# Kernel tuning notes

Measured on AMD Instinct MI355X. Metric: run time of the kernel, lower is better.

The kernel has to match this reference:

```python
import jax, jax.numpy as jnp
import numpy as np

N_NODES = 50000
N_EDGES = 800000
N_REL = 8
DIM = 256


def setup_inputs() -> dict:
    key = jax.random.key(0)
    ks = jax.random.split(key, 6)
    x = jax.random.normal(ks[0], (N_NODES, DIM), dtype=jnp.float32)
    # xavier-uniform-ish scale for [R, in, out] weights
    limit = float(np.sqrt(6.0 / (DIM + DIM)))
    W0 = jax.random.uniform(ks[1], (N_REL, DIM, DIM), dtype=jnp.float32, minval=-limit, maxval=limit)
    W1 = jax.random.uniform(ks[2], (N_REL, DIM, DIM), dtype=jnp.float32, minval=-limit, maxval=limit)
    b0 = jnp.zeros((DIM,), dtype=jnp.float32)
    b1 = jnp.zeros((DIM,), dtype=jnp.float32)
    edge_index = jax.random.randint(ks[3], (2, N_EDGES), 0, N_NODES, dtype=jnp.int64)
    edge_type = jax.random.randint(ks[4], (N_EDGES,), 0, N_REL, dtype=jnp.int64)
    return {"x": x, "W0": W0, "b0": b0, "W1": W1, "b1": b1,
            "edge_index": edge_index, "edge_type": edge_type}


def _rgcn_layer(x, W, b, src, dst, edge_type, num_nodes):
    # grouped GEMM over all relations: [R, N, out]
    xt = jnp.einsum('ni,rio->rno', x, W)
    # per-edge message = relu(x[src] @ W[edge_type] + b)  -> [E, out]
    msg = jax.nn.relu(xt[edge_type, src] + b)
    # scatter-add into destination nodes
    return jax.ops.segment_sum(msg, dst, num_segments=num_nodes)


def reference(x, W0, b0, W1, b1, edge_index, edge_type):
    src, dst = edge_index[0], edge_index[1]
    h = _rgcn_layer(x, W0, b0, src, dst, edge_type, x.shape[0])
    h = _rgcn_layer(h, W1, b1, src, dst, edge_type, x.shape[0])
    return h
```

## Files before the change

### kernel.cpp

```cpp
#include <hip/hip_runtime.h>

#define DIM 256
#define N_REL 8

typedef __attribute__((ext_vector_type(8))) short short8_t;
typedef __attribute__((ext_vector_type(4))) float float4_t;

__device__ inline unsigned short f2bf(float f) {
    unsigned u = __float_as_uint(f);
    u += 0x7FFFu + ((u >> 16) & 1u);
    return (unsigned short)(u >> 16);
}
__device__ inline float bf2f(unsigned short h) {
    return __uint_as_float(((unsigned)h) << 16);
}

__global__ __launch_bounds__(256) void cast_f32_bf16(
    const float* __restrict__ in, unsigned short* __restrict__ out, int n4)
{
    const int i = blockIdx.x * blockDim.x + threadIdx.x;
    if (i >= n4) return;
    const float4 v = ((const float4*)in)[i];
    ushort4 o;
    o.x = f2bf(v.x); o.y = f2bf(v.y); o.z = f2bf(v.z); o.w = f2bf(v.w);
    ((ushort4*)out)[i] = o;
}

__global__ __launch_bounds__(256) void transpose_cast_w(
    const float* __restrict__ W, unsigned short* __restrict__ Wt)
{
    __shared__ float tile[32][33];
    const int rel = blockIdx.z;
    const int i0 = blockIdx.x * 32, o0 = blockIdx.y * 32;
    const int tx = threadIdx.x, ty = threadIdx.y;
    const float* Wr = W + (size_t)rel * DIM * DIM;
    unsigned short* Wtr = Wt + (size_t)rel * DIM * DIM;
#pragma unroll
    for (int j = 0; j < 4; j++)
        tile[ty + 8 * j][tx] = Wr[(size_t)(i0 + ty + 8 * j) * DIM + o0 + tx];
    __syncthreads();
#pragma unroll
    for (int j = 0; j < 4; j++)
        Wtr[(size_t)(o0 + ty + 8 * j) * DIM + i0 + tx] = f2bf(tile[tx][ty + 8 * j]);
}

__global__ __launch_bounds__(256) void gemm_mfma_bias_relu(
    const unsigned short* __restrict__ Xb,
    const unsigned short* __restrict__ Wtb,
    const float* __restrict__ bias,
    unsigned short* __restrict__ Yall, int M, int Rtiles)
{
    __shared__ __align__(16) short smem[16384];

    const unsigned L = blockIdx.x;
    const int xcd = L & 7;
    const unsigned g = L >> 3;
    const int combo = g & 15;
    const int rt = (int)((g >> 4) << 3) | xcd;
    if (rt >= Rtiles) return;
    const int m0 = rt * 128;
    const int n0 = (combo & 1) * 128;
    const int rel = combo >> 1;

    const unsigned short* Wt = Wtb + (size_t)rel * DIM * DIM;
    unsigned short* Y = Yall + (size_t)rel * M * DIM;

    const int t = threadIdx.x;
    const int lane = t & 63;
    const int w = t >> 6;
    const int wr = w & 1, wc = w >> 1;
    const int r = lane & 15, q = lane >> 4;

    const int sl = lane & 3;
    const int rsub = lane >> 2;
    const unsigned short* gA[2];
    const unsigned short* gB[2];
#pragma unroll
    for (int h = 0; h < 2; h++) {
        const int row = h * 64 + w * 16 + rsub;
        const int gseg = sl ^ ((row >> 1) & 3);
        gA[h] = Xb + (size_t)(m0 + row) * DIM + gseg * 8;
        gB[h] = Wt + (size_t)(n0 + row) * DIM + gseg * 8;
    }

    const int swz = (q ^ ((r >> 1) & 3)) * 8;
    int offA[4], offB[4];
#pragma unroll
    for (int mi = 0; mi < 4; mi++)
        offA[mi] = (wr * 64 + mi * 16 + r) * 32 + swz;
#pragma unroll
    for (int ni = 0; ni < 4; ni++)
        offB[ni] = (wc * 64 + ni * 16 + r) * 32 + swz;

    float4_t acc[4][4];
#pragma unroll
    for (int i = 0; i < 4; i++)
#pragma unroll
        for (int j = 0; j < 4; j++) {
            float4_t z = {0.f, 0.f, 0.f, 0.f};
            acc[i][j] = z;
        }

#define STAGE(ks, bsel)                                                         \
    {                                                                           \
        const int k0_ = (ks) * 32;                                              \
        short* Ad_ = smem + ((bsel) ? 8192 : 0);                                \
        short* Bd_ = Ad_ + 4096;                                                \
        _Pragma("unroll")                                                       \
        for (int h = 0; h < 2; h++) {                                           \
            __builtin_amdgcn_global_load_lds(                                   \
                (const __attribute__((address_space(1))) unsigned int*)(gA[h] + k0_), \
                (__attribute__((address_space(3))) unsigned int*)(Ad_ + h * 2048 + w * 512), \
                16, 0, 0);                                                      \
            __builtin_amdgcn_global_load_lds(                                   \
                (const __attribute__((address_space(1))) unsigned int*)(gB[h] + k0_), \
                (__attribute__((address_space(3))) unsigned int*)(Bd_ + h * 2048 + w * 512), \
                16, 0, 0);                                                      \
        }                                                                       \
    }

    STAGE(0, 0);
#pragma unroll 1
    for (int ks = 0; ks < 8; ks++) {
        const int cur = ks & 1;
        if (ks < 7) {
            STAGE(ks + 1, cur ^ 1);
            asm volatile("s_waitcnt vmcnt(4)" ::: "memory");
        } else {
            asm volatile("s_waitcnt vmcnt(0)" ::: "memory");
        }
        asm volatile("s_barrier" ::: "memory");

        const short* As_b = smem + (cur ? 8192 : 0);
        const short* Bs_b = As_b + 4096;
        short8_t af[4], bf[4];
#pragma unroll
        for (int mi = 0; mi < 4; mi++)
            af[mi] = *(const short8_t*)&As_b[offA[mi]];
#pragma unroll
        for (int ni = 0; ni < 4; ni++)
            bf[ni] = *(const short8_t*)&Bs_b[offB[ni]];
#pragma unroll
        for (int mi = 0; mi < 4; mi++)
#pragma unroll
            for (int ni = 0; ni < 4; ni++)
                acc[mi][ni] = __builtin_amdgcn_mfma_f32_16x16x32_bf16(
                    af[mi], bf[ni], acc[mi][ni], 0, 0, 0);
        asm volatile("s_barrier" ::: "memory");
    }
#undef STAGE

    short* St = smem;

    float bv[4];
#pragma unroll
    for (int ni = 0; ni < 4; ni++)
        bv[ni] = bias[n0 + wc * 64 + ni * 16 + r];

#pragma unroll
    for (int mi = 0; mi < 4; mi++) {
#pragma unroll
        for (int ni = 0; ni < 4; ni++) {
#pragma unroll
            for (int e = 0; e < 4; e++) {
                const int rl = wr * 16 + q * 4 + e;
                const int col = wc * 64 + ni * 16 + r;
                St[rl * 136 + col] = f2bf(fmaxf(acc[mi][ni][e] + bv[ni], 0.f));
            }
        }
        __syncthreads();
#pragma unroll
        for (int j = 0; j < 2; j++) {
            const int id = t + 256 * j;
            const int rl = id >> 4;
            const int ch = id & 15;
            const int grow = m0 + (rl >> 4) * 64 + mi * 16 + (rl & 15);
            const short8_t v = *(const short8_t*)&St[rl * 136 + ch * 8];
            if (grow < M)
                *(short8_t*)&Y[(size_t)grow * DIM + n0 + ch * 8] = v;
        }
        __syncthreads();
    }
}

__global__ __launch_bounds__(256) void count_dst(
    const int* __restrict__ dst, int E, int* __restrict__ cnt)
{
    const int e = blockIdx.x * blockDim.x + threadIdx.x;
    if (e < E) atomicAdd(&cnt[dst[e]], 1);
}

__global__ __launch_bounds__(256) void scan_blocksums(
    const int* __restrict__ cnt, int N, int* __restrict__ bsum)
{
    __shared__ int red[256];
    const int t = threadIdx.x;
    const int base = blockIdx.x * 1024 + t * 4;
    int s = 0;
#pragma unroll
    for (int j = 0; j < 4; j++) {
        const int i = base + j;
        if (i < N) s += cnt[i];
    }
    red[t] = s;
    __syncthreads();
#pragma unroll
    for (int off = 128; off > 0; off >>= 1) {
        if (t < off) red[t] += red[t + off];
        __syncthreads();
    }
    if (t == 0) bsum[blockIdx.x] = red[0];
}

__global__ __launch_bounds__(256) void scan_offsets(
    int* __restrict__ bsum, int nb, int* __restrict__ rowptr, int N)
{
    __shared__ int sh[256];
    const int t = threadIdx.x;
    sh[t] = (t < nb) ? bsum[t] : 0;
    __syncthreads();
    for (int off = 1; off < 256; off <<= 1) {
        const int add = (t >= off) ? sh[t - off] : 0;
        __syncthreads();
        sh[t] += add;
        __syncthreads();
    }
    if (t < nb) bsum[t] = (t == 0) ? 0 : sh[t - 1];
    if (t == 255) rowptr[N] = sh[255];
}

__global__ __launch_bounds__(256) void scan_phase3(
    const int* __restrict__ cnt, int N, const int* __restrict__ bsum,
    int* __restrict__ rowptr, int* __restrict__ cursor)
{
    __shared__ int sh[256];
    const int t = threadIdx.x;
    const int base = blockIdx.x * 1024 + t * 4;
    int v[4];
#pragma unroll
    for (int j = 0; j < 4; j++) {
        const int i = base + j;
        v[j] = (i < N) ? cnt[i] : 0;
    }
    sh[t] = v[0] + v[1] + v[2] + v[3];
    __syncthreads();
    for (int off = 1; off < 256; off <<= 1) {
        const int add = (t >= off) ? sh[t - off] : 0;
        __syncthreads();
        sh[t] += add;
        __syncthreads();
    }
    int run = bsum[blockIdx.x] + ((t == 0) ? 0 : sh[t - 1]);
#pragma unroll
    for (int j = 0; j < 4; j++) {
        const int i = base + j;
        if (i < N) { rowptr[i] = run; cursor[i] = run; }
        run += v[j];
    }
}

__global__ __launch_bounds__(256) void fill_edges(
    const int* __restrict__ src, const int* __restrict__ dst,
    const int* __restrict__ et, int E, int* __restrict__ cursor,
    unsigned* __restrict__ ep)
{
    const int e = blockIdx.x * blockDim.x + threadIdx.x;
    if (e >= E) return;
    const int pos = atomicAdd(&cursor[dst[e]], 1);
    ep[pos] = (unsigned)src[e] | ((unsigned)et[e] << 16);
}

template <typename OT>
__global__ __launch_bounds__(256) void aggregate4(
    const unsigned short* __restrict__ yall,
    const unsigned* __restrict__ ep, const int* __restrict__ rowptr,
    OT* __restrict__ out, int M)
{
    const int lane = threadIdx.x & 63;
    const int half = lane >> 5;
    const int cl = lane & 31;
    const int wv = (blockIdx.x * blockDim.x + threadIdx.x) >> 6;
    const int nw = (gridDim.x * blockDim.x) >> 6;
    const size_t plane = (size_t)M * DIM;

    for (int d = wv; d < M; d += nw) {
        const int beg = rowptr[d], end = rowptr[d + 1];
        float acc[8];
#pragma unroll
        for (int j = 0; j < 8; j++) acc[j] = 0.f;

        for (int c0 = beg; c0 < end; c0 += 64) {
            const int n = min(64, end - c0);
            const unsigned myep = (c0 + lane < end) ? ep[c0 + lane] : 0u;
            for (int i = 0; i < n; i += 4) {
                const int i0 = i + half;
                const int i1 = i + 2 + half;
                const unsigned p0 = __shfl(myep, i0 & 63);
                const unsigned p1 = __shfl(myep, i1 & 63);
                const short8_t u0 = *(const short8_t*)(
                    yall + (size_t)(p0 >> 16) * plane +
                    (size_t)(p0 & 0xFFFFu) * DIM + cl * 8);
                const short8_t u1 = *(const short8_t*)(
                    yall + (size_t)(p1 >> 16) * plane +
                    (size_t)(p1 & 0xFFFFu) * DIM + cl * 8);
                if (i0 < n) {
#pragma unroll
                    for (int j = 0; j < 8; j++)
                        acc[j] += bf2f((unsigned short)u0[j]);
                }
                if (i1 < n) {
#pragma unroll
                    for (int j = 0; j < 8; j++)
                        acc[j] += bf2f((unsigned short)u1[j]);
                }
            }
        }
        float o[8];
#pragma unroll
        for (int j = 0; j < 8; j++)
            o[j] = acc[j] + __shfl(acc[j], (lane + 32) & 63);
        if (lane < 32) {
            OT* dp = out + (size_t)d * DIM + cl * 8;
            if (sizeof(OT) == 4) {
                *(float4*)((float*)dp) = make_float4(o[0], o[1], o[2], o[3]);
                *(float4*)((float*)dp + 4) = make_float4(o[4], o[5], o[6], o[7]);
            } else {
                short8_t v;
#pragma unroll
                for (int j = 0; j < 8; j++) v[j] = (short)f2bf(o[j]);
                *(short8_t*)((unsigned short*)dp) = v;
            }
        }
    }
}

__global__ __launch_bounds__(256) void gemm_bias_relu_f32(
    const float* __restrict__ A, const float* __restrict__ B,
    const float* __restrict__ bias, float* __restrict__ Y, int M)
{
    __shared__ float Asf[16][132];
    __shared__ float Bsf[16][128];
    const int t = threadIdx.x;
    const int tx = t & 15, ty = t >> 4;
    const int row0 = blockIdx.x * 128, col0 = blockIdx.y * 128;
    float acc[8][8];
#pragma unroll
    for (int i = 0; i < 8; i++)
#pragma unroll
        for (int j = 0; j < 8; j++) acc[i][j] = 0.f;
    const int arow = t >> 2, akseg = (t & 3) * 4;
    const int bk0 = t >> 5, bcol = (t & 31) * 4;
    for (int k0 = 0; k0 < DIM; k0 += 16) {
#pragma unroll
        for (int h = 0; h < 2; h++) {
            const int row = row0 + arow + h * 64;
            float4 av = (row < M) ? *(const float4*)(A + (size_t)row * DIM + k0 + akseg)
                                  : make_float4(0, 0, 0, 0);
            Asf[akseg + 0][arow + h * 64] = av.x;
            Asf[akseg + 1][arow + h * 64] = av.y;
            Asf[akseg + 2][arow + h * 64] = av.z;
            Asf[akseg + 3][arow + h * 64] = av.w;
        }
#pragma unroll
        for (int h = 0; h < 2; h++) {
            const int krow = bk0 + h * 8;
            *(float4*)&Bsf[krow][bcol] =
                *(const float4*)(B + (size_t)(k0 + krow) * DIM + col0 + bcol);
        }
        __syncthreads();
#pragma unroll
        for (int k = 0; k < 16; k++) {
            float a[8], b[8];
            *(float4*)&a[0] = *(const float4*)&Asf[k][ty * 4];
            *(float4*)&a[4] = *(const float4*)&Asf[k][64 + ty * 4];
            *(float4*)&b[0] = *(const float4*)&Bsf[k][tx * 4];
            *(float4*)&b[4] = *(const float4*)&Bsf[k][64 + tx * 4];
#pragma unroll
            for (int i = 0; i < 8; i++)
#pragma unroll
                for (int j = 0; j < 8; j++) acc[i][j] = fmaf(a[i], b[j], acc[i][j]);
        }
        __syncthreads();
    }
#pragma unroll
    for (int im = 0; im < 2; im++)
#pragma unroll
        for (int i = 0; i < 4; i++) {
            const int row = row0 + im * 64 + ty * 4 + i;
            if (row >= M) continue;
#pragma unroll
            for (int jm = 0; jm < 2; jm++) {
                const int col = col0 + jm * 64 + tx * 4;
                const float4 bb = *(const float4*)(bias + col);
                float4 o;
                o.x = fmaxf(acc[im * 4 + i][jm * 4 + 0] + bb.x, 0.f);
                o.y = fmaxf(acc[im * 4 + i][jm * 4 + 1] + bb.y, 0.f);
                o.z = fmaxf(acc[im * 4 + i][jm * 4 + 2] + bb.z, 0.f);
                o.w = fmaxf(acc[im * 4 + i][jm * 4 + 3] + bb.w, 0.f);
                *(float4*)(Y + (size_t)row * DIM + col) = o;
            }
        }
}

__global__ __launch_bounds__(256) void scatter_rel(
    const float* __restrict__ y, const int* __restrict__ src,
    const int* __restrict__ dst, const int* __restrict__ et,
    int rel, float* __restrict__ out, int n_edges)
{
    const int lane = threadIdx.x & 63;
    const int wave = (blockIdx.x * blockDim.x + threadIdx.x) >> 6;
    const int nwaves = (gridDim.x * blockDim.x) >> 6;
    for (int e = wave; e < n_edges; e += nwaves) {
        if (et[e] != rel) continue;
        const float4 v = *(const float4*)(y + (size_t)src[e] * DIM + lane * 4);
        float* o = out + (size_t)dst[e] * DIM + lane * 4;
        atomicAdd(o + 0, v.x);
        atomicAdd(o + 1, v.y);
        atomicAdd(o + 2, v.z);
        atomicAdd(o + 3, v.w);
    }
}

static inline size_t align16(size_t x) { return (x + 15) & ~(size_t)15; }

extern "C" void kernel_launch(void* const* d_in, const int* in_sizes, int n_in,
                              void* d_out, int out_size, void* d_ws, size_t ws_size,
                              hipStream_t stream)
{
    const float* x  = (const float*)d_in[0];
    const float* W0 = (const float*)d_in[1];
    const float* b0 = (const float*)d_in[2];
    const float* W1 = (const float*)d_in[3];
    const float* b1 = (const float*)d_in[4];
    const int* eidx = (const int*)d_in[5];
    const int* etyp = (const int*)d_in[6];

    const int M = in_sizes[0] / DIM;
    const int E = in_sizes[6];
    const int* src = eidx;
    const int* dst = eidx + E;
    float* out = (float*)d_out;

    const size_t plane = (size_t)M * DIM;
    const size_t wbytes = (size_t)N_REL * DIM * DIM * 2;

    const size_t need = align16(plane * 2)
                      + align16(plane * 2)
                      + 2 * align16(wbytes)
                      + align16((size_t)(M + 1) * 4)
                      + 2 * align16((size_t)M * 4)
                      + align16((size_t)256 * 4)
                      + align16((size_t)E * 4)
                      + align16((size_t)N_REL * plane * 2);

    if (M < 65536 && ws_size >= need) {
        char* ws = (char*)d_ws;
        size_t off = 0;
        unsigned short* h1b  = (unsigned short*)(ws + off); off = align16(off + plane * 2);
        unsigned short* xb   = (unsigned short*)(ws + off); off = align16(off + plane * 2);
        unsigned short* Wt0b = (unsigned short*)(ws + off); off = align16(off + wbytes);
        unsigned short* Wt1b = (unsigned short*)(ws + off); off = align16(off + wbytes);
        int* rowptr = (int*)(ws + off); off = align16(off + (size_t)(M + 1) * 4);
        int* cnt    = (int*)(ws + off); off = align16(off + (size_t)M * 4);
        int* cursor = (int*)(ws + off); off = align16(off + (size_t)M * 4);
        int* bsum   = (int*)(ws + off); off = align16(off + (size_t)256 * 4);
        unsigned* ep = (unsigned*)(ws + off); off = align16(off + (size_t)E * 4);
        unsigned short* yall = (unsigned short*)(ws + off);

        const int nb = (M + 1023) / 1024;
        hipMemsetAsync(cnt, 0, (size_t)M * 4, stream);
        count_dst<<<(E + 255) / 256, 256, 0, stream>>>(dst, E, cnt);
        scan_blocksums<<<nb, 256, 0, stream>>>(cnt, M, bsum);
        scan_offsets<<<1, 256, 0, stream>>>(bsum, nb, rowptr, M);
        scan_phase3<<<nb, 256, 0, stream>>>(cnt, M, bsum, rowptr, cursor);
        fill_edges<<<(E + 255) / 256, 256, 0, stream>>>(src, dst, etyp, E, cursor, ep);

        cast_f32_bf16<<<(int)((plane / 4 + 255) / 256), 256, 0, stream>>>(
            x, xb, (int)(plane / 4));
        transpose_cast_w<<<dim3(8, 8, N_REL), dim3(32, 8), 0, stream>>>(W0, Wt0b);
        transpose_cast_w<<<dim3(8, 8, N_REL), dim3(32, 8), 0, stream>>>(W1, Wt1b);

        const int Rtiles = (M + 127) / 128;
        const int octets = (Rtiles + 7) / 8;
        const int ggrid = octets * 16 * 8;
        const int agrid = (int)(((size_t)M * 64 + 255) / 256);

        gemm_mfma_bias_relu<<<ggrid, 256, 0, stream>>>(xb, Wt0b, b0, yall, M, Rtiles);
        aggregate4<unsigned short><<<agrid, 256, 0, stream>>>(yall, ep, rowptr, h1b, M);
        gemm_mfma_bias_relu<<<ggrid, 256, 0, stream>>>(h1b, Wt1b, b1, yall, M, Rtiles);
        aggregate4<float><<<agrid, 256, 0, stream>>>(yall, ep, rowptr, out, M);
    } else {
        float* h1 = (float*)d_ws;
        float* y  = (float*)d_ws + plane;
        const dim3 gblk(256), ggrid2((M + 127) / 128, DIM / 128);
        hipMemsetAsync(h1, 0, plane * 4, stream);
        for (int r = 0; r < N_REL; r++) {
            gemm_bias_relu_f32<<<ggrid2, gblk, 0, stream>>>(
                x, W0 + (size_t)r * DIM * DIM, b0, y, M);
            scatter_rel<<<1024, 256, 0, stream>>>(y, src, dst, etyp, r, h1, E);
        }
        hipMemsetAsync(out, 0, plane * 4, stream);
        for (int r = 0; r < N_REL; r++) {
            gemm_bias_relu_f32<<<ggrid2, gblk, 0, stream>>>(
                h1, W1 + (size_t)r * DIM * DIM, b1, y, M);
            scatter_rel<<<1024, 256, 0, stream>>>(y, src, dst, etyp, r, out, E);
        }
    }
}
```

Baseline: 510.0 us.

## Triple-buffer GEMM LDS pipeline, batch epilogue stores, deepen gather loads

The GEMM K-loop moves from double to triple buffering in LDS with two stages prefetched ahead, and the loop is fully unrolled. The aim is to hide more global-load latency behind the MFMAs. The epilogue now writes two 16-row slices per barrier pair, which halves the number of __syncthreads. The CSR gather loop issues four independent row loads per iteration instead of two, raising memory-level parallelism. The costs are more LDS per block, which may lower occupancy, and higher register pressure.

```diff
diff --git a/kernel.cpp b/kernel.cpp
--- a/kernel.cpp
+++ b/kernel.cpp
@@ -50,7 +50,7 @@
     const float* __restrict__ bias,
     unsigned short* __restrict__ Yall, int M, int Rtiles)
 {
-    __shared__ __align__(16) short smem[16384];
+    __shared__ __align__(16) short smem[24576];
 
     const unsigned L = blockIdx.x;
     const int xcd = L & 7;
@@ -104,7 +104,7 @@
 #define STAGE(ks, bsel)                                                         \
     {                                                                           \
         const int k0_ = (ks) * 32;                                              \
-        short* Ad_ = smem + ((bsel) ? 8192 : 0);                                \
+        short* Ad_ = smem + (bsel) * 8192;                                      \
         short* Bd_ = Ad_ + 4096;                                                \
         _Pragma("unroll")                                                       \
         for (int h = 0; h < 2; h++) {                                           \
@@ -120,18 +120,20 @@
     }
 
     STAGE(0, 0);
-#pragma unroll 1
+    STAGE(1, 1);
+#pragma unroll
     for (int ks = 0; ks < 8; ks++) {
-        const int cur = ks & 1;
-        if (ks < 7) {
-            STAGE(ks + 1, cur ^ 1);
+        if (ks < 6) {
+            STAGE(ks + 2, (ks + 2) % 3);
+            asm volatile("s_waitcnt vmcnt(8)" ::: "memory");
+        } else if (ks == 6) {
             asm volatile("s_waitcnt vmcnt(4)" ::: "memory");
         } else {
             asm volatile("s_waitcnt vmcnt(0)" ::: "memory");
         }
         asm volatile("s_barrier" ::: "memory");
 
-        const short* As_b = smem + (cur ? 8192 : 0);
+        const short* As_b = smem + (ks % 3) * 8192;
         const short* Bs_b = As_b + 4096;
         short8_t af[4], bf[4];
 #pragma unroll
@@ -158,28 +160,34 @@
         bv[ni] = bias[n0 + wc * 64 + ni * 16 + r];
 
 #pragma unroll
-    for (int mi = 0; mi < 4; mi++) {
-#pragma unroll
-        for (int ni = 0; ni < 4; ni++) {
-#pragma unroll
-            for (int e = 0; e < 4; e++) {
-                const int rl = wr * 16 + q * 4 + e;
-                const int col = wc * 64 + ni * 16 + r;
-                St[rl * 136 + col] = f2bf(fmaxf(acc[mi][ni][e] + bv[ni], 0.f));
+    for (int mp = 0; mp < 2; mp++) {
+#pragma unroll
+        for (int s = 0; s < 2; s++) {
+#pragma unroll
+            for (int ni = 0; ni < 4; ni++) {
+#pragma unroll
+                for (int e = 0; e < 4; e++) {
+                    const int rl = s * 32 + wr * 16 + q * 4 + e;
+                    const int col = wc * 64 + ni * 16 + r;
+                    St[rl * 136 + col] =
+                        f2bf(fmaxf(acc[mp * 2 + s][ni][e] + bv[ni], 0.f));
+                }
             }
         }
         __syncthreads();
 #pragma unroll
-        for (int j = 0; j < 2; j++) {
+        for (int j = 0; j < 4; j++) {
             const int id = t + 256 * j;
-            const int rl = id >> 4;
+            const int rl2 = id >> 4;
             const int ch = id & 15;
-            const int grow = m0 + (rl >> 4) * 64 + mi * 16 + (rl & 15);
-            const short8_t v = *(const short8_t*)&St[rl * 136 + ch * 8];
+            const int s = rl2 >> 5;
+            const int rl = rl2 & 31;
+            const int grow = m0 + (rl >> 4) * 64 + (mp * 2 + s) * 16 + (rl & 15);
+            const short8_t v = *(const short8_t*)&St[rl2 * 136 + ch * 8];
             if (grow < M)
                 *(short8_t*)&Y[(size_t)grow * DIM + n0 + ch * 8] = v;
         }
-        __syncthreads();
+        if (mp == 0) __syncthreads();
     }
 }
 
@@ -292,26 +300,22 @@
         for (int c0 = beg; c0 < end; c0 += 64) {
             const int n = min(64, end - c0);
             const unsigned myep = (c0 + lane < end) ? ep[c0 + lane] : 0u;
-            for (int i = 0; i < n; i += 4) {
-                const int i0 = i + half;
-                const int i1 = i + 2 + half;
-                const unsigned p0 = __shfl(myep, i0 & 63);
-                const unsigned p1 = __shfl(myep, i1 & 63);
-                const short8_t u0 = *(const short8_t*)(
-                    yall + (size_t)(p0 >> 16) * plane +
-                    (size_t)(p0 & 0xFFFFu) * DIM + cl * 8);
-                const short8_t u1 = *(const short8_t*)(
-                    yall + (size_t)(p1 >> 16) * plane +
-                    (size_t)(p1 & 0xFFFFu) * DIM + cl * 8);
-                if (i0 < n) {
-#pragma unroll
-                    for (int j = 0; j < 8; j++)
-                        acc[j] += bf2f((unsigned short)u0[j]);
+            for (int i = 0; i < n; i += 8) {
+                short8_t u[4];
+#pragma unroll
+                for (int j = 0; j < 4; j++) {
+                    const unsigned p = __shfl(myep, (i + 2 * j + half) & 63);
+                    u[j] = *(const short8_t*)(
+                        yall + (size_t)(p >> 16) * plane +
+                        (size_t)(p & 0xFFFFu) * DIM + cl * 8);
                 }
-                if (i1 < n) {
-#pragma unroll
-                    for (int j = 0; j < 8; j++)
-                        acc[j] += bf2f((unsigned short)u1[j]);
+#pragma unroll
+                for (int j = 0; j < 4; j++) {
+                    if (i + 2 * j + half < n) {
+#pragma unroll
+                        for (int k = 0; k < 8; k++)
+                            acc[k] += bf2f((unsigned short)u[j][k]);
+                    }
                 }
             }
         }
```

Measured after the change: 508.7 us. Within noise of the previous version (-0.2%).
